# Kernel optimization log

Measured on AMD Instinct MI355X. Metric: run time of the kernel, lower is better.

Reference implementation:

```python
import jax, jax.numpy as jnp
import numpy as np

H = 256          # hidden_size
L = 131072       # encoder sequence length
CE = PE = DE = 10
CHORDS, PITCHES, DURS = 158, 63, 16
IN = CE + PE + DE + CE + CE  # 50 = chord + pitch + dur + sec + context
S = 0.05


def setup_inputs() -> dict:
    key = jax.random.key(0)
    k = jax.random.split(key, 16)
    return {
        "sec": 3,
        "chord": 7,
        "true_pitch": 12,
        "note": jax.random.randint(k[0], (2,), 0, 16),
        "hn": jax.random.normal(k[1], (1, 1, H), jnp.float32) * S,
        "cn": jax.random.normal(k[2], (1, 1, H), jnp.float32) * S,
        "encoder_outputs": jax.random.normal(k[3], (L, H), jnp.float32) * S,
        "chord_emb": jax.random.normal(k[4], (CHORDS, CE), jnp.float32) * S,
        "pitch_emb": jax.random.normal(k[5], (PITCHES, PE), jnp.float32) * S,
        "dur_emb": jax.random.normal(k[6], (DURS, DE), jnp.float32) * S,
        "W_ih": jax.random.normal(k[7], (4 * H, IN), jnp.float32) * S,
        "W_hh": jax.random.normal(k[8], (4 * H, H), jnp.float32) * S,
        "b_ih": jax.random.normal(k[9], (4 * H,), jnp.float32) * S,
        "b_hh": jax.random.normal(k[10], (4 * H,), jnp.float32) * S,
        "pitch_W": jax.random.normal(k[11], (PITCHES, H), jnp.float32) * S,
        "pitch_b": jax.random.normal(k[12], (PITCHES,), jnp.float32) * S,
        "dur_W": jax.random.normal(k[13], (DURS, PE + H), jnp.float32) * S,
        "dur_b": jax.random.normal(k[14], (DURS,), jnp.float32) * S,
        "attn_W": jax.random.normal(k[15], (CE, H), jnp.float32) * S,
        "attn_b": jnp.zeros((CE,), jnp.float32),
    }


def reference(sec, chord, true_pitch, note, hn, cn, encoder_outputs,
              chord_emb, pitch_emb, dur_emb, W_ih, W_hh, b_ih, b_hh,
              pitch_W, pitch_b, dur_W, dur_b, attn_W, attn_b):
    h = hn.reshape(-1)  # [H]
    c = cn.reshape(-1)  # [H]

    # embedding lookups
    e_chord = chord_emb[chord]        # [10]
    e_sec = chord_emb[sec]            # [10]
    e_pitch = pitch_emb[note[0]]      # [10]
    e_dur = dur_emb[note[1]]          # [10]
    e_true = pitch_emb[true_pitch]    # [10]

    # dot-product attention over encoder_outputs (vectorized version of the loop)
    scores = encoder_outputs @ h              # [L]
    w = jax.nn.softmax(scores)                # [L]
    ctx = w @ encoder_outputs                 # [H]
    ctx = ctx @ attn_W.T + attn_b             # [10]

    # single-step LSTM (PyTorch gate order i, f, g, o)
    x = jnp.concatenate([e_pitch, e_dur, e_chord, e_sec, ctx])  # [50]
    gates = W_ih @ x + W_hh @ h + b_ih + b_hh                   # [4H]
    i_g, f_g, g_g, o_g = jnp.split(gates, 4)
    i_g = jax.nn.sigmoid(i_g)
    f_g = jax.nn.sigmoid(f_g)
    g_g = jnp.tanh(g_g)
    o_g = jax.nn.sigmoid(o_g)
    c_new = f_g * c + i_g * g_g
    h_new = o_g * jnp.tanh(c_new)

    # dual heads
    pitch_out = (h_new @ pitch_W.T + pitch_b)[None, :]                      # [1,63]
    dur_out = (jnp.concatenate([e_true, h_new]) @ dur_W.T + dur_b)[None, :]  # [1,16]

    return pitch_out, dur_out, h_new.reshape(1, 1, H), c_new.reshape(1, 1, H)
```

## Files before the change

kernel.cpp:

```cpp
#include <hip/hip_runtime.h>
#include <hip/hip_bf16.h>
#include <math.h>

#define H 256
#define L_SEQ 131072
#define NBLK 1024
#define RPB (L_SEQ / NBLK)

__device__ __forceinline__ float wave_reduce_sum(float v) {
#pragma unroll
  for (int off = 32; off > 0; off >>= 1) v += __shfl_xor(v, off, 64);
  return v;
}

__global__ __launch_bounds__(256, 4) void k1_attn(
    const float* __restrict__ E, const float* __restrict__ h,
    const float* __restrict__ attn_W, const float* __restrict__ W_hh,
    const float* __restrict__ b_ih, const float* __restrict__ b_hh,
    const float* __restrict__ W_ih,
    const float* __restrict__ chord_emb, const float* __restrict__ pitch_emb,
    const float* __restrict__ dur_emb,
    const int* __restrict__ sec_p, const int* __restrict__ chord_p,
    const int* __restrict__ note_p,
    const float* __restrict__ pitch_W, const float* __restrict__ dur_W,
    float* __restrict__ p10, float* __restrict__ ghh2,
    float* __restrict__ WcT, float* __restrict__ dummy) {
  const int b = blockIdx.x;
  const int t = threadIdx.x;
  const int lane = t & 63;
  const int w = t >> 6;
  const float4 hreg = reinterpret_cast<const float4*>(h)[lane];

  float s = 0.f;
  float4 acc = make_float4(0.f, 0.f, 0.f, 0.f);
  const float4* E4 = reinterpret_cast<const float4*>(E);
  const size_t base = (size_t)b * RPB;
#pragma unroll
  for (int k = 0; k < RPB / 32; ++k) {
    const int r = w * 8 + 32 * k;
    float4 e[8];
#pragma unroll
    for (int j = 0; j < 8; ++j) e[j] = E4[(base + r + j) * 64 + lane];
    float d[8];
#pragma unroll
    for (int j = 0; j < 8; ++j)
      d[j] = e[j].x * hreg.x + e[j].y * hreg.y + e[j].z * hreg.z + e[j].w * hreg.w;
#pragma unroll
    for (int off = 32; off > 0; off >>= 1) {
#pragma unroll
      for (int j = 0; j < 8; ++j) d[j] += __shfl_xor(d[j], off, 64);
    }
#pragma unroll
    for (int j = 0; j < 8; ++j) {
      const float wj = __expf(d[j]);
      s += wj;
      acc.x += wj * e[j].x;
      acc.y += wj * e[j].y;
      acc.z += wj * e[j].z;
      acc.w += wj * e[j].w;
    }
  }
  __shared__ float ss[4];
  __shared__ float4 sacc4[4][64];
  sacc4[w][lane] = acc;
  if (lane == 0) ss[w] = s;
  __syncthreads();
  __shared__ float ctx_s[H];
  {
    const float* sf = reinterpret_cast<const float*>(sacc4);
    ctx_s[t] = (sf[t] + sf[256 + t]) + (sf[512 + t] + sf[768 + t]);
  }
  __syncthreads();
  const float4 c4 = reinterpret_cast<const float4*>(ctx_s)[lane];
  for (int row = w; row < 10; row += 4) {
    const float4 a4 = reinterpret_cast<const float4*>(attn_W + row * H)[lane];
    float d = c4.x * a4.x + c4.y * a4.y + c4.z * a4.z + c4.w * a4.w;
    d = wave_reduce_sum(d);
    if (lane == 0) p10[row * NBLK + b] = d;
  }
  if (t == 0) p10[10 * NBLK + b] = (ss[0] + ss[1]) + (ss[2] + ss[3]);

  if (b < 256) {
    const int r = b * 4 + w;
    const float4 wv = reinterpret_cast<const float4*>(W_hh + (size_t)r * H)[lane];
    float d = wv.x * hreg.x + wv.y * hreg.y + wv.z * hreg.z + wv.w * hreg.w;
    if (lane < 50) {
      const float wih = W_ih[r * 50 + lane];
      if (lane < 40) {
        int idx; const float* tbl;
        if (lane < 10)      { tbl = pitch_emb; idx = note_p[0] * 10 + lane; }
        else if (lane < 20) { tbl = dur_emb;   idx = note_p[1] * 10 + lane - 10; }
        else if (lane < 30) { tbl = chord_emb; idx = chord_p[0] * 10 + lane - 20; }
        else                { tbl = chord_emb; idx = sec_p[0] * 10 + lane - 30; }
        d += wih * tbl[idx];
      } else {
        WcT[(lane - 40) * NBLK + r] = wih;
      }
    }
    d = wave_reduce_sum(d);
    if (lane == 0) ghh2[r] = d + b_ih[r] + b_hh[r];
  } else if (b < 272) {
    const int slice = b - 256;
    float a = 0.f;
    const float4* pw4 = reinterpret_cast<const float4*>(pitch_W);
    for (int i = slice * 256 + t; i < 4032; i += 16 * 256) {
      float4 v = pw4[i]; a += v.x + v.y + v.z + v.w;
    }
    const float4* dw4 = reinterpret_cast<const float4*>(dur_W);
    for (int i = slice * 256 + t; i < 1064; i += 16 * 256) {
      float4 v = dw4[i]; a += v.x + v.y + v.z + v.w;
    }
    a = wave_reduce_sum(a);
    if (lane == 0) dummy[slice * 4 + w] = a;
  }
}

__global__ __launch_bounds__(1024) void k2_tail(
    const float* __restrict__ p10, const float* __restrict__ ghh2,
    const float* __restrict__ WcT, const float* __restrict__ attn_b,
    const float* __restrict__ c_in,
    const float* __restrict__ pitch_W, const float* __restrict__ pitch_b,
    const float* __restrict__ dur_W, const float* __restrict__ dur_b,
    const float* __restrict__ pitch_emb, const int* __restrict__ tp_p,
    float* __restrict__ out) {
  const int t = threadIdx.x;
  const int lane = t & 63, w = t >> 6;
  __shared__ float red[11];
  __shared__ float ctxsh[10];
  __shared__ float gsh[1024];
  __shared__ float hsh[H];
  __shared__ float etsh[10];
  if (w < 11) {
    const float4* pc = reinterpret_cast<const float4*>(p10 + w * NBLK);
    const float4 a0 = pc[lane], a1 = pc[lane + 64];
    const float4 a2 = pc[lane + 128], a3 = pc[lane + 192];
    float v = (a0.x + a0.y + a0.z + a0.w) + (a1.x + a1.y + a1.z + a1.w) +
              (a2.x + a2.y + a2.z + a2.w) + (a3.x + a3.y + a3.z + a3.w);
    v = wave_reduce_sum(v);
    if (lane == 0) red[w] = v;
  }
  if (t >= 704 && t < 714) etsh[t - 704] = pitch_emb[tp_p[0] * 10 + (t - 704)];
  __syncthreads();
  if (t < 10) ctxsh[t] = red[t] / red[10] + attn_b[t];
  __syncthreads();
  float g = ghh2[t];
#pragma unroll
  for (int c = 0; c < 10; c++) g += WcT[c * NBLK + t] * ctxsh[c];
  gsh[t] = g;
  __syncthreads();
  if (t < H) {
    const float i_s = 1.f / (1.f + __expf(-gsh[t]));
    const float f_s = 1.f / (1.f + __expf(-gsh[256 + t]));
    const float g_t = tanhf(gsh[512 + t]);
    const float o_s = 1.f / (1.f + __expf(-gsh[768 + t]));
    const float cn = f_s * c_in[t] + i_s * g_t;
    const float hn = o_s * tanhf(cn);
    if (blockIdx.x == 0) {
      out[79 + t] = hn;
      out[335 + t] = cn;
    }
    hsh[t] = hn;
  }
  __syncthreads();
  const int gw = blockIdx.x * 16 + w;
  const float4 h4 = reinterpret_cast<const float4*>(hsh)[lane];
  if (gw < 63) {
    const float4 pw = reinterpret_cast<const float4*>(pitch_W + (size_t)gw * H)[lane];
    float d = pw.x * h4.x + pw.y * h4.y + pw.z * h4.z + pw.w * h4.w;
    d = wave_reduce_sum(d);
    if (lane == 0) out[gw] = d + pitch_b[gw];
  }
  if (gw >= 48) {
    const int row = gw - 48;
    const float* dw = dur_W + (size_t)row * 266;
    float d = 0.f;
    for (int k = lane; k < 266; k += 64)
      d += dw[k] * (k < 10 ? etsh[k] : hsh[k - 10]);
    d = wave_reduce_sum(d);
    if (lane == 0) out[63 + row] = d + dur_b[row];
  }
}

extern "C" void kernel_launch(void* const* d_in, const int* in_sizes, int n_in,
                              void* d_out, int out_size, void* d_ws, size_t ws_size,
                              hipStream_t stream) {
  const int* sec       = (const int*)d_in[0];
  const int* chord     = (const int*)d_in[1];
  const int* tp        = (const int*)d_in[2];
  const int* note      = (const int*)d_in[3];
  const float* hn      = (const float*)d_in[4];
  const float* cn      = (const float*)d_in[5];
  const float* E       = (const float*)d_in[6];
  const float* chord_e = (const float*)d_in[7];
  const float* pitch_e = (const float*)d_in[8];
  const float* dur_e   = (const float*)d_in[9];
  const float* W_ih    = (const float*)d_in[10];
  const float* W_hh    = (const float*)d_in[11];
  const float* b_ih    = (const float*)d_in[12];
  const float* b_hh    = (const float*)d_in[13];
  const float* pitch_W = (const float*)d_in[14];
  const float* pitch_b = (const float*)d_in[15];
  const float* dur_W   = (const float*)d_in[16];
  const float* dur_b   = (const float*)d_in[17];
  const float* attn_W  = (const float*)d_in[18];
  const float* attn_b  = (const float*)d_in[19];
  float* out = (float*)d_out;
  float* ws = (float*)d_ws;

  float* p10   = ws;
  float* ghh2  = ws + 11 * NBLK;
  float* WcT   = ghh2 + 1024;
  float* dummy = WcT + 10 * NBLK;

  k1_attn<<<NBLK, 256, 0, stream>>>(E, hn, attn_W, W_hh, b_ih, b_hh, W_ih,
                                    chord_e, pitch_e, dur_e, sec, chord, note,
                                    pitch_W, dur_W, p10, ghh2, WcT, dummy);
  k2_tail<<<4, 1024, 0, stream>>>(p10, ghh2, WcT, attn_b, cn,
                                  pitch_W, pitch_b, dur_W, dur_b,
                                  pitch_e, tp, out);
}
```

Before: 32.12 us.

## Fuse tail into attention kernel via last-block atomic counter; use nontemporal loads

Merges the second tail kernel into the main attention kernel. Each block increments a global counter after writing its partials, and the last block to finish performs the softmax normalization, LSTM gates and output heads. This removes a kernel launch and the gap between the two kernels. Encoder loads are switched to nontemporal loads to avoid polluting the cache. The tail now runs on a single 256-thread block instead of four 1024-thread blocks, and the counter relies on modulo wraparound because it is never reset.

```diff
diff --git a/kernel.cpp b/kernel.cpp
--- a/kernel.cpp
+++ b/kernel.cpp
@@ -7,13 +7,15 @@
 #define NBLK 1024
 #define RPB (L_SEQ / NBLK)
 
+typedef __attribute__((ext_vector_type(4))) float f32x4;
+
 __device__ __forceinline__ float wave_reduce_sum(float v) {
 #pragma unroll
   for (int off = 32; off > 0; off >>= 1) v += __shfl_xor(v, off, 64);
   return v;
 }
 
-__global__ __launch_bounds__(256, 4) void k1_attn(
+__global__ __launch_bounds__(256, 4) void k1_fused(
     const float* __restrict__ E, const float* __restrict__ h,
     const float* __restrict__ attn_W, const float* __restrict__ W_hh,
     const float* __restrict__ b_ih, const float* __restrict__ b_hh,
@@ -21,10 +23,13 @@
     const float* __restrict__ chord_emb, const float* __restrict__ pitch_emb,
     const float* __restrict__ dur_emb,
     const int* __restrict__ sec_p, const int* __restrict__ chord_p,
-    const int* __restrict__ note_p,
-    const float* __restrict__ pitch_W, const float* __restrict__ dur_W,
+    const int* __restrict__ tp_p, const int* __restrict__ note_p,
+    const float* __restrict__ attn_b, const float* __restrict__ c_in,
+    const float* __restrict__ pitch_W, const float* __restrict__ pitch_b,
+    const float* __restrict__ dur_W, const float* __restrict__ dur_b,
     float* __restrict__ p10, float* __restrict__ ghh2,
-    float* __restrict__ WcT, float* __restrict__ dummy) {
+    float* __restrict__ WcT, float* __restrict__ dummy,
+    unsigned* __restrict__ cnt, float* __restrict__ out) {
   const int b = blockIdx.x;
   const int t = threadIdx.x;
   const int lane = t & 63;
@@ -33,14 +38,15 @@
 
   float s = 0.f;
   float4 acc = make_float4(0.f, 0.f, 0.f, 0.f);
-  const float4* E4 = reinterpret_cast<const float4*>(E);
+  const f32x4* E4 = reinterpret_cast<const f32x4*>(E);
   const size_t base = (size_t)b * RPB;
 #pragma unroll
   for (int k = 0; k < RPB / 32; ++k) {
     const int r = w * 8 + 32 * k;
-    float4 e[8];
-#pragma unroll
-    for (int j = 0; j < 8; ++j) e[j] = E4[(base + r + j) * 64 + lane];
+    f32x4 e[8];
+#pragma unroll
+    for (int j = 0; j < 8; ++j)
+      e[j] = __builtin_nontemporal_load(&E4[(base + r + j) * 64 + lane]);
     float d[8];
 #pragma unroll
     for (int j = 0; j < 8; ++j)
@@ -71,12 +77,14 @@
     ctx_s[t] = (sf[t] + sf[256 + t]) + (sf[512 + t] + sf[768 + t]);
   }
   __syncthreads();
-  const float4 c4 = reinterpret_cast<const float4*>(ctx_s)[lane];
-  for (int row = w; row < 10; row += 4) {
-    const float4 a4 = reinterpret_cast<const float4*>(attn_W + row * H)[lane];
-    float d = c4.x * a4.x + c4.y * a4.y + c4.z * a4.z + c4.w * a4.w;
-    d = wave_reduce_sum(d);
-    if (lane == 0) p10[row * NBLK + b] = d;
+  {
+    const float4 c4 = reinterpret_cast<const float4*>(ctx_s)[lane];
+    for (int row = w; row < 10; row += 4) {
+      const float4 a4 = reinterpret_cast<const float4*>(attn_W + row * H)[lane];
+      float d = c4.x * a4.x + c4.y * a4.y + c4.z * a4.z + c4.w * a4.w;
+      d = wave_reduce_sum(d);
+      if (lane == 0) p10[row * NBLK + b] = d;
+    }
   }
   if (t == 0) p10[10 * NBLK + b] = (ss[0] + ss[1]) + (ss[2] + ss[3]);
 
@@ -113,65 +121,68 @@
     a = wave_reduce_sum(a);
     if (lane == 0) dummy[slice * 4 + w] = a;
   }
-}
-
-__global__ __launch_bounds__(1024) void k2_tail(
-    const float* __restrict__ p10, const float* __restrict__ ghh2,
-    const float* __restrict__ WcT, const float* __restrict__ attn_b,
-    const float* __restrict__ c_in,
-    const float* __restrict__ pitch_W, const float* __restrict__ pitch_b,
-    const float* __restrict__ dur_W, const float* __restrict__ dur_b,
-    const float* __restrict__ pitch_emb, const int* __restrict__ tp_p,
-    float* __restrict__ out) {
-  const int t = threadIdx.x;
-  const int lane = t & 63, w = t >> 6;
+
+  __syncthreads();
+  __shared__ unsigned oldsh;
+  if (t == 0) {
+    __threadfence();
+    oldsh = __hip_atomic_fetch_add(cnt, 1u, __ATOMIC_ACQ_REL,
+                                   __HIP_MEMORY_SCOPE_AGENT);
+  }
+  __syncthreads();
+  if ((oldsh & (NBLK - 1u)) != (NBLK - 1u)) return;
+  if (t == 0) __threadfence();
+  __syncthreads();
+
   __shared__ float red[11];
   __shared__ float ctxsh[10];
   __shared__ float gsh[1024];
   __shared__ float hsh[H];
-  __shared__ float etsh[10];
-  if (w < 11) {
-    const float4* pc = reinterpret_cast<const float4*>(p10 + w * NBLK);
-    const float4 a0 = pc[lane], a1 = pc[lane + 64];
-    const float4 a2 = pc[lane + 128], a3 = pc[lane + 192];
-    float v = (a0.x + a0.y + a0.z + a0.w) + (a1.x + a1.y + a1.z + a1.w) +
-              (a2.x + a2.y + a2.z + a2.w) + (a3.x + a3.y + a3.z + a3.w);
+  __shared__ float etsh[16];
+  for (int col = w; col < 11; col += 4) {
+    const float4* pc = reinterpret_cast<const float4*>(p10 + col * NBLK);
+    float v = 0.f;
+#pragma unroll
+    for (int i = 0; i < 4; ++i) {
+      const float4 a = pc[lane + 64 * i];
+      v += (a.x + a.y) + (a.z + a.w);
+    }
     v = wave_reduce_sum(v);
-    if (lane == 0) red[w] = v;
-  }
-  if (t >= 704 && t < 714) etsh[t - 704] = pitch_emb[tp_p[0] * 10 + (t - 704)];
+    if (lane == 0) red[col] = v;
+  }
+  if (t < 10) etsh[t] = pitch_emb[tp_p[0] * 10 + t];
   __syncthreads();
   if (t < 10) ctxsh[t] = red[t] / red[10] + attn_b[t];
   __syncthreads();
-  float g = ghh2[t];
-#pragma unroll
-  for (int c = 0; c < 10; c++) g += WcT[c * NBLK + t] * ctxsh[c];
-  gsh[t] = g;
-  __syncthreads();
-  if (t < H) {
+#pragma unroll
+  for (int i = 0; i < 4; ++i) {
+    const int r = t + 256 * i;
+    float g = ghh2[r];
+#pragma unroll
+    for (int c = 0; c < 10; ++c) g += WcT[c * NBLK + r] * ctxsh[c];
+    gsh[r] = g;
+  }
+  __syncthreads();
+  {
     const float i_s = 1.f / (1.f + __expf(-gsh[t]));
     const float f_s = 1.f / (1.f + __expf(-gsh[256 + t]));
     const float g_t = tanhf(gsh[512 + t]);
     const float o_s = 1.f / (1.f + __expf(-gsh[768 + t]));
     const float cn = f_s * c_in[t] + i_s * g_t;
     const float hn = o_s * tanhf(cn);
-    if (blockIdx.x == 0) {
-      out[79 + t] = hn;
-      out[335 + t] = cn;
-    }
+    out[79 + t] = hn;
+    out[335 + t] = cn;
     hsh[t] = hn;
   }
   __syncthreads();
-  const int gw = blockIdx.x * 16 + w;
   const float4 h4 = reinterpret_cast<const float4*>(hsh)[lane];
-  if (gw < 63) {
-    const float4 pw = reinterpret_cast<const float4*>(pitch_W + (size_t)gw * H)[lane];
+  for (int row = w; row < 63; row += 4) {
+    const float4 pw = reinterpret_cast<const float4*>(pitch_W + (size_t)row * H)[lane];
     float d = pw.x * h4.x + pw.y * h4.y + pw.z * h4.z + pw.w * h4.w;
     d = wave_reduce_sum(d);
-    if (lane == 0) out[gw] = d + pitch_b[gw];
-  }
-  if (gw >= 48) {
-    const int row = gw - 48;
+    if (lane == 0) out[row] = d + pitch_b[row];
+  }
+  for (int row = w; row < 16; row += 4) {
     const float* dw = dur_W + (size_t)row * 266;
     float d = 0.f;
     for (int k = lane; k < 266; k += 64)
@@ -207,15 +218,15 @@
   float* out = (float*)d_out;
   float* ws = (float*)d_ws;
 
-  float* p10   = ws;
-  float* ghh2  = ws + 11 * NBLK;
-  float* WcT   = ghh2 + 1024;
-  float* dummy = WcT + 10 * NBLK;
-
-  k1_attn<<<NBLK, 256, 0, stream>>>(E, hn, attn_W, W_hh, b_ih, b_hh, W_ih,
-                                    chord_e, pitch_e, dur_e, sec, chord, note,
-                                    pitch_W, dur_W, p10, ghh2, WcT, dummy);
-  k2_tail<<<4, 1024, 0, stream>>>(p10, ghh2, WcT, attn_b, cn,
-                                  pitch_W, pitch_b, dur_W, dur_b,
-                                  pitch_e, tp, out);
+  float* p10      = ws;
+  float* ghh2     = ws + 11 * NBLK;
+  float* WcT      = ghh2 + 1024;
+  float* dummy    = WcT + 10 * NBLK;
+  unsigned* cnt   = (unsigned*)(dummy + 64);
+
+  k1_fused<<<NBLK, 256, 0, stream>>>(E, hn, attn_W, W_hh, b_ih, b_hh, W_ih,
+                                     chord_e, pitch_e, dur_e, sec, chord, tp,
+                                     note, attn_b, cn, pitch_W, pitch_b,
+                                     dur_W, dur_b, p10, ghh2, WcT, dummy,
+                                     cnt, out);
 }
```

After: 73.21 us. 2.28x slower.
